# Optimization experiments

Hardware: AMD Instinct MI355X
Metric: run time of the kernel (lower is better)

Reference implementation:

```python
import jax, jax.numpy as jnp
import numpy as np

TEMP = 0.07
NEG_INF = -1e30  # finite stand-in for -inf; safe under vjp


def setup_inputs() -> dict:
    key = jax.random.key(0)
    k1, k2, k3 = jax.random.split(key, 3)
    B, D, H, F = 16384, 2048, 2048, 128  # 2N rows, backbone_dim, hidden_dim, feature_dim
    features = jax.random.normal(k1, (B, D), dtype=jnp.float32)
    w1 = jax.random.normal(k2, (D, H), dtype=jnp.float32) / np.sqrt(D)
    b1 = jnp.zeros((H,), dtype=jnp.float32)
    w2 = jax.random.normal(k3, (H, F), dtype=jnp.float32) / np.sqrt(H)
    b2 = jnp.zeros((F,), dtype=jnp.float32)
    return {"features": features, "w1": w1, "b1": b1, "w2": w2, "b2": b2}


def reference(features, w1, b1, w2, b2):
    # Projector: Linear -> ReLU -> Linear, then L2-normalize (F.normalize, dim=1)
    h = jax.nn.relu(features @ w1 + b1)
    p = h @ w2 + b2
    z = p / jnp.maximum(jnp.linalg.norm(p, axis=1, keepdims=True), 1e-12)

    M = z.shape[0]           # 2N
    N = M // 2
    sim = (z @ z.T) / TEMP   # [2N, 2N]

    # NT-Xent with labels=0: loss_i = logsumexp_{j != i}(sim[i,j]) - pos_i
    # (pos appears exactly once among the logits, so the gather loop over
    #  per-row negatives collapses to a diagonal-masked row logsumexp).
    diag = jnp.eye(M, dtype=bool)
    lse = jax.nn.logsumexp(jnp.where(diag, NEG_INF, sim), axis=1)
    pos = jnp.sum(z * jnp.roll(z, N, axis=0), axis=1) / TEMP  # sim[i, (i+N) % 2N]
    loss = jnp.mean(lse - pos)
    return loss, z[:N], z[N:]
```

## Files before the change

### kernel.cpp

```cpp
#include <hip/hip_runtime.h>

typedef __attribute__((ext_vector_type(8))) __bf16 bf16x8;
typedef __attribute__((ext_vector_type(4))) float f32x4;

#define B_ROWS 16384
#define N_HALF 8192
#define D_DIM  2048
#define H_DIM  2048
#define F_DIM  128

static constexpr float kInvT = 14.285714285714286f;
static constexpr float kS2   = 20.60992915555662f;

__device__ __forceinline__ void async16(void* lds, const void* g) {
  __builtin_amdgcn_global_load_lds((const __attribute__((address_space(1))) void*)g,
                                   (__attribute__((address_space(3))) void*)lds,
                                   16, 0, 0);
}

__global__ void cvt_bf16_kernel(const float* __restrict__ in, __bf16* __restrict__ out, int n) {
  int i = (blockIdx.x * blockDim.x + threadIdx.x) * 8;
  if (i >= n) return;
  float4 a = *(const float4*)(in + i);
  float4 b = *(const float4*)(in + i + 4);
  bf16x8 o;
  o[0] = (__bf16)a.x; o[1] = (__bf16)a.y; o[2] = (__bf16)a.z; o[3] = (__bf16)a.w;
  o[4] = (__bf16)b.x; o[5] = (__bf16)b.y; o[6] = (__bf16)b.z; o[7] = (__bf16)b.w;
  *(bf16x8*)(out + i) = o;
}

__global__ void transpose_cvt_kernel(const float* __restrict__ in, __bf16* __restrict__ out,
                                     int R, int C) {
  __shared__ float tile[32][33];
  int tx = threadIdx.x, ty = threadIdx.y;
  int c0 = blockIdx.x * 32, r0 = blockIdx.y * 32;
  for (int i = 0; i < 4; i++)
    tile[ty + i * 8][tx] = in[(size_t)(r0 + ty + i * 8) * C + c0 + tx];
  __syncthreads();
  for (int i = 0; i < 4; i++)
    out[(size_t)(c0 + ty + i * 8) * R + r0 + tx] = (__bf16)tile[tx][ty + i * 8];
}

#define BM 256
#define BK 64
#define NT_K (D_DIM / BK)

__global__ __launch_bounds__(512, 2) void gemm1_8ph_kernel(
    const __bf16* __restrict__ A, const __bf16* __restrict__ BT,
    const float* __restrict__ bias, __bf16* __restrict__ C) {
  __shared__ __align__(16) __bf16 As[2][BM * BK];
  __shared__ __align__(16) __bf16 Bs[2][BM * BK];
  const int t = threadIdx.x;
  const int wave = t >> 6, lane = t & 63;
  const int l15 = lane & 15, quad = lane >> 4, l7 = l15 & 7;
  const int wy = wave & 1, wx = wave >> 1;

  const int wg = ((int)blockIdx.x & 7) * 64 + ((int)blockIdx.x >> 3);
  const int n0 = (wg & 7) * 256;
  const int m0 = (wg >> 3) * 256;

  const int tr = t >> 3;
  const int csw = ((t & 7) ^ (tr & 7)) * 8;
  const __bf16* pA = A + (size_t)(m0 + tr) * D_DIM + csw;
  const __bf16* pB = BT + (size_t)(n0 + tr) * D_DIM + csw;
  const int ldsw = wave * 512;

  auto stageA = [&](int buf, int h, int kk) {
    async16(&As[buf][h * 8192 + ldsw], pA + (size_t)(h * 128) * D_DIM + kk);
    async16(&As[buf][h * 8192 + 4096 + ldsw], pA + (size_t)(h * 128 + 64) * D_DIM + kk);
  };
  auto stageB = [&](int buf, int h, int kk) {
    async16(&Bs[buf][h * 8192 + ldsw], pB + (size_t)(h * 128) * D_DIM + kk);
    async16(&Bs[buf][h * 8192 + 4096 + ldsw], pB + (size_t)(h * 128 + 64) * D_DIM + kk);
  };

  const int arow = wy * 16 + l15;
  const int brow = wx * 16 + l15;
  const int s0 = (quad ^ l7) * 8;
  const int s1 = ((4 + quad) ^ l7) * 8;

  f32x4 acc[8][4];
#pragma unroll
  for (int f = 0; f < 8; f++)
#pragma unroll
    for (int n = 0; n < 4; n++) acc[f][n] = 0.f;

  stageB(0, 0, 0); stageB(0, 1, 0);
  stageA(0, 0, 0); stageA(0, 1, 0);
  stageB(1, 0, BK); stageB(1, 1, BK);
  asm volatile("s_waitcnt vmcnt(4)" ::: "memory");
  __builtin_amdgcn_s_barrier();

  for (int tk = 0; tk < NT_K; ++tk) {
    const int cur = tk & 1, nxt = cur ^ 1;
    const __bf16* Ac = &As[cur][0];
    const __bf16* Bc = &Bs[cur][0];
#define LDA(f, s) (*(const bf16x8*)(Ac + ((f) * 32 + arow) * 64 + (s)))
#define LDB(n, s) (*(const bf16x8*)(Bc + ((n) * 64 + brow) * 64 + (s)))
    bf16x8 b0[4], b1[4];
    {
      bf16x8 a0 = LDA(0, s0), a1 = LDA(1, s0), a2 = LDA(2, s0), a3 = LDA(3, s0);
      b0[0] = LDB(0, s0); b0[1] = LDB(1, s0); b0[2] = LDB(2, s0); b0[3] = LDB(3, s0);
      if (tk + 1 < NT_K) stageA(nxt, 0, (tk + 1) * BK);
      __builtin_amdgcn_s_barrier();
      asm volatile("s_waitcnt lgkmcnt(0)" ::: "memory");
      __builtin_amdgcn_s_setprio(1);
#pragma unroll
      for (int n = 0; n < 4; n++) {
        acc[0][n] = __builtin_amdgcn_mfma_f32_16x16x32_bf16(a0, b0[n], acc[0][n], 0, 0, 0);
        acc[1][n] = __builtin_amdgcn_mfma_f32_16x16x32_bf16(a1, b0[n], acc[1][n], 0, 0, 0);
        acc[2][n] = __builtin_amdgcn_mfma_f32_16x16x32_bf16(a2, b0[n], acc[2][n], 0, 0, 0);
        acc[3][n] = __builtin_amdgcn_mfma_f32_16x16x32_bf16(a3, b0[n], acc[3][n], 0, 0, 0);
      }
      __builtin_amdgcn_s_setprio(0);
      __builtin_amdgcn_s_barrier();
    }
    {
      bf16x8 a4 = LDA(4, s0), a5 = LDA(5, s0), a6 = LDA(6, s0), a7 = LDA(7, s0);
      if (tk + 1 < NT_K) stageA(nxt, 1, (tk + 1) * BK);
      __builtin_amdgcn_s_barrier();
      asm volatile("s_waitcnt lgkmcnt(0)" ::: "memory");
      __builtin_amdgcn_s_setprio(1);
#pragma unroll
      for (int n = 0; n < 4; n++) {
        acc[4][n] = __builtin_amdgcn_mfma_f32_16x16x32_bf16(a4, b0[n], acc[4][n], 0, 0, 0);
        acc[5][n] = __builtin_amdgcn_mfma_f32_16x16x32_bf16(a5, b0[n], acc[5][n], 0, 0, 0);
        acc[6][n] = __builtin_amdgcn_mfma_f32_16x16x32_bf16(a6, b0[n], acc[6][n], 0, 0, 0);
        acc[7][n] = __builtin_amdgcn_mfma_f32_16x16x32_bf16(a7, b0[n], acc[7][n], 0, 0, 0);
      }
      __builtin_amdgcn_s_setprio(0);
      __builtin_amdgcn_s_barrier();
    }
    {
      bf16x8 a0 = LDA(0, s1), a1 = LDA(1, s1), a2 = LDA(2, s1), a3 = LDA(3, s1);
      b1[0] = LDB(0, s1); b1[1] = LDB(1, s1); b1[2] = LDB(2, s1); b1[3] = LDB(3, s1);
      __builtin_amdgcn_s_barrier();
      asm volatile("s_waitcnt lgkmcnt(0)" ::: "memory");
      __builtin_amdgcn_s_setprio(1);
#pragma unroll
      for (int n = 0; n < 4; n++) {
        acc[0][n] = __builtin_amdgcn_mfma_f32_16x16x32_bf16(a0, b1[n], acc[0][n], 0, 0, 0);
        acc[1][n] = __builtin_amdgcn_mfma_f32_16x16x32_bf16(a1, b1[n], acc[1][n], 0, 0, 0);
        acc[2][n] = __builtin_amdgcn_mfma_f32_16x16x32_bf16(a2, b1[n], acc[2][n], 0, 0, 0);
        acc[3][n] = __builtin_amdgcn_mfma_f32_16x16x32_bf16(a3, b1[n], acc[3][n], 0, 0, 0);
      }
      __builtin_amdgcn_s_setprio(0);
      __builtin_amdgcn_s_barrier();
    }
    {
      bf16x8 a4 = LDA(4, s1), a5 = LDA(5, s1), a6 = LDA(6, s1), a7 = LDA(7, s1);
      if (tk + 2 < NT_K) {
        stageB(cur, 0, (tk + 2) * BK);
        stageB(cur, 1, (tk + 2) * BK);
        asm volatile("s_waitcnt vmcnt(4)" ::: "memory");
      } else if (tk + 1 < NT_K) {
        asm volatile("s_waitcnt vmcnt(0)" ::: "memory");
      }
      __builtin_amdgcn_s_barrier();
      asm volatile("s_waitcnt lgkmcnt(0)" ::: "memory");
      __builtin_amdgcn_s_setprio(1);
#pragma unroll
      for (int n = 0; n < 4; n++) {
        acc[4][n] = __builtin_amdgcn_mfma_f32_16x16x32_bf16(a4, b1[n], acc[4][n], 0, 0, 0);
        acc[5][n] = __builtin_amdgcn_mfma_f32_16x16x32_bf16(a5, b1[n], acc[5][n], 0, 0, 0);
        acc[6][n] = __builtin_amdgcn_mfma_f32_16x16x32_bf16(a6, b1[n], acc[6][n], 0, 0, 0);
        acc[7][n] = __builtin_amdgcn_mfma_f32_16x16x32_bf16(a7, b1[n], acc[7][n], 0, 0, 0);
      }
      __builtin_amdgcn_s_setprio(0);
      __builtin_amdgcn_s_barrier();
    }
#undef LDA
#undef LDB
  }

#pragma unroll
  for (int n = 0; n < 4; n++) {
    int col = n0 + n * 64 + wx * 16 + l15;
    float bv = bias[col];
#pragma unroll
    for (int f = 0; f < 8; f++) {
      int rowb = m0 + f * 32 + wy * 16 + quad * 4;
#pragma unroll
      for (int r = 0; r < 4; r++) {
        float v = fmaxf(acc[f][n][r] + bv, 0.f);
        C[(size_t)(rowb + r) * H_DIM + col] = (__bf16)v;
      }
    }
  }
}

__global__ __launch_bounds__(256) void proj_norm_kernel(
    const __bf16* __restrict__ A, const __bf16* __restrict__ BT,
    const float* __restrict__ bias, float* __restrict__ zf, __bf16* __restrict__ zb, int K) {
  __shared__ __align__(16) __bf16 As[64 * 32];
  __shared__ __align__(16) __bf16 Bs[128 * 32];
  __shared__ float pbuf[64 * 128];
  const int t = threadIdx.x;
  const int wave = t >> 6, lane = t & 63;
  const int l15 = lane & 15, quad = lane >> 4;
  const int wy = wave >> 1, wx = wave & 1;
  const int m0 = blockIdx.x * 64;
  const int sr = t >> 2;
  const int sk = (((t & 3) ^ ((sr >> 1) & 3))) * 8;
  const int sw = (l15 >> 1) & 3;

  f32x4 acc[2][4];
  for (int i = 0; i < 2; i++)
    for (int j = 0; j < 4; j++) acc[i][j] = 0.f;

  for (int k0 = 0; k0 < K; k0 += 32) {
    async16(As + wave * 512, A + (size_t)(m0 + sr) * K + k0 + sk);
    async16(Bs + 0 * 2048 + wave * 512, BT + (size_t)(0  + sr) * K + k0 + sk);
    async16(Bs + 1 * 2048 + wave * 512, BT + (size_t)(64 + sr) * K + k0 + sk);
    __syncthreads();
    bf16x8 af[2], bfr[4];
    for (int i = 0; i < 2; i++)
      af[i] = *(const bf16x8*)(As + (wy * 32 + i * 16 + l15) * 32 + (quad ^ sw) * 8);
    for (int i = 0; i < 4; i++)
      bfr[i] = *(const bf16x8*)(Bs + (wx * 64 + i * 16 + l15) * 32 + (quad ^ sw) * 8);
    for (int mi = 0; mi < 2; mi++)
      for (int ni = 0; ni < 4; ni++)
        acc[mi][ni] = __builtin_amdgcn_mfma_f32_16x16x32_bf16(af[mi], bfr[ni], acc[mi][ni], 0, 0, 0);
    __syncthreads();
  }
  for (int ni = 0; ni < 4; ni++) {
    int col = wx * 64 + ni * 16 + l15;
    float bv = bias[col];
    for (int mi = 0; mi < 2; mi++) {
      int lrow = wy * 32 + mi * 16 + quad * 4;
      for (int r = 0; r < 4; r++)
        pbuf[(lrow + r) * 128 + col] = acc[mi][ni][r] + bv;
    }
  }
  __syncthreads();
  for (int it = 0; it < 16; it++) {
    int lrow = wave * 16 + it;
    float v0 = pbuf[lrow * 128 + lane];
    float v1 = pbuf[lrow * 128 + 64 + lane];
    float ss = v0 * v0 + v1 * v1;
    for (int m = 1; m < 64; m <<= 1) ss += __shfl_xor(ss, m);
    float inv = 1.f / fmaxf(sqrtf(ss), 1e-12f);
    float z0 = v0 * inv, z1 = v1 * inv;
    size_t base = (size_t)(m0 + lrow) * F_DIM;
    zf[base + lane] = z0;
    zf[base + 64 + lane] = z1;
    zb[base + lane] = (__bf16)z0;
    zb[base + 64 + lane] = (__bf16)z1;
  }
}

__global__ __launch_bounds__(256) void sim_lse_tri_kernel(const __bf16* __restrict__ zb,
                                                          float* __restrict__ S,
                                                          float* __restrict__ colpart) {
  __shared__ __align__(16) __bf16 Bs[128 * 128];
  const int t = threadIdx.x;
  const int wave = t >> 6, lane = t & 63;
  const int l15 = lane & 15, quad = lane >> 4;
  const int wy = wave >> 1, wx = wave & 1;
  const int srow = t >> 4;
  const int schunk = (t & 15) ^ srow;

  const int u = blockIdx.x * 8;
  auto fr = [](int r) { return r * 128 - (r * (r - 1)) / 2; };
  int rt = (int)(128.5f - sqrtf(16512.25f - 2.0f * (float)u));
  while (fr(rt + 1) <= u) rt++;
  while (fr(rt) > u) rt--;
  int ct = rt + (u - fr(rt));

  bf16x8 a[4][4];
  float rowacc[4][4];
  auto load_a = [&](int rtile) {
#pragma unroll
    for (int mi = 0; mi < 4; mi++)
#pragma unroll
      for (int ks = 0; ks < 4; ks++)
        a[mi][ks] = *(const bf16x8*)(zb + (size_t)(rtile * 128 + wy * 64 + mi * 16 + l15) * 128 +
                                     ks * 32 + quad * 8);
  };
  auto flush_rows = [&](int rtile) {
#pragma unroll
    for (int mi = 0; mi < 4; mi++)
#pragma unroll
      for (int r = 0; r < 4; r++) {
        float v = rowacc[mi][r];
        v += __shfl_xor(v, 1);
        v += __shfl_xor(v, 2);
        v += __shfl_xor(v, 4);
        v += __shfl_xor(v, 8);
        if (l15 == 0)
          atomicAdd(&S[rtile * 128 + wy * 64 + mi * 16 + quad * 4 + r], v);
        rowacc[mi][r] = 0.f;
      }
  };

#pragma unroll
  for (int mi = 0; mi < 4; mi++)
#pragma unroll
    for (int r = 0; r < 4; r++) rowacc[mi][r] = 0.f;
  load_a(rt);

  for (int it = 0; it < 8; ++it) {
    const __bf16* gbase = zb + (size_t)(ct * 128) * 128;
#pragma unroll
    for (int q = 0; q < 8; q++)
      async16(Bs + q * 2048 + wave * 512, gbase + (size_t)(q * 16 + srow) * 128 + schunk * 8);
    __syncthreads();
    const bool diag = (ct == rt);
#pragma unroll
    for (int ni = 0; ni < 4; ni++) {
      bf16x8 b[4];
      const int brow = wx * 64 + ni * 16 + l15;
#pragma unroll
      for (int ks = 0; ks < 4; ks++)
        b[ks] = *(const bf16x8*)(Bs + brow * 128 + (((ks * 4 + quad) ^ l15) * 8));
      float colsum = 0.f;
      if (diag) {
#pragma unroll
        for (int mi = 0; mi < 4; mi++) {
          f32x4 acc = 0.f;
#pragma unroll
          for (int ks = 0; ks < 4; ks++)
            acc = __builtin_amdgcn_mfma_f32_16x16x32_bf16(a[mi][ks], b[ks], acc, 0, 0, 0);
          const int lrb = wy * 64 + mi * 16 + quad * 4;
#pragma unroll
          for (int r = 0; r < 4; r++) {
            float term = __builtin_amdgcn_exp2f(fmaf(acc[r], kS2, -kS2));
            rowacc[mi][r] += (lrb + r == brow) ? 0.f : term;
          }
        }
      } else {
#pragma unroll
        for (int mi = 0; mi < 4; mi++) {
          f32x4 acc = 0.f;
#pragma unroll
          for (int ks = 0; ks < 4; ks++)
            acc = __builtin_amdgcn_mfma_f32_16x16x32_bf16(a[mi][ks], b[ks], acc, 0, 0, 0);
#pragma unroll
          for (int r = 0; r < 4; r++) {
            float term = __builtin_amdgcn_exp2f(fmaf(acc[r], kS2, -kS2));
            rowacc[mi][r] += term;
            colsum += term;
          }
        }
        colsum += __shfl_xor(colsum, 16);
        colsum += __shfl_xor(colsum, 32);
        if (quad == 0)
          colpart[((size_t)(ct * 128 + rt) * 2 + wy) * 128 + brow] = colsum;
      }
    }
    __syncthreads();
    if (it < 7) {
      ct++;
      if (ct == 128) {
        flush_rows(rt);
        rt++;
        ct = rt;
        load_a(rt);
      }
    }
  }
  flush_rows(rt);
}

__global__ __launch_bounds__(128) void col_reduce_kernel(const float* __restrict__ colpart,
                                                         float* __restrict__ S) {
  const int ct = blockIdx.y;
  const int r0 = blockIdx.x * 32;
  if (r0 >= ct) return;
  const int t = threadIdx.x;
  const int rend = min(ct, r0 + 32);
  float s = 0.f;
  for (int rt = r0; rt < rend; rt++) {
    const float* p = colpart + (size_t)(ct * 128 + rt) * 2 * 128;
    s += p[t] + p[128 + t];
  }
  atomicAdd(&S[ct * 128 + t], s);
}

__global__ void loss_kernel(const float* __restrict__ zf, const float* __restrict__ S,
                            float* __restrict__ out) {
  int wave = threadIdx.x >> 6, lane = threadIdx.x & 63;
  int base = blockIdx.x * 64 + wave * 16;
  float local = 0.f;
  for (int it = 0; it < 16; it++) {
    int row = base + it;
    int j = (row + N_HALF) & (B_ROWS - 1);
    const float* za = zf + (size_t)row * F_DIM;
    const float* zc = zf + (size_t)j * F_DIM;
    float d = za[lane] * zc[lane] + za[lane + 64] * zc[lane + 64];
    for (int m = 1; m < 64; m <<= 1) d += __shfl_xor(d, m);
    float pos = d * kInvT;
    float lse = logf(S[row]) + kInvT;
    local += (lse - pos);
  }
  if (lane == 0) atomicAdd(out, local * (1.f / B_ROWS));
}

extern "C" void kernel_launch(void* const* d_in, const int* in_sizes, int n_in,
                              void* d_out, int out_size, void* d_ws, size_t ws_size,
                              hipStream_t stream) {
  const float* features = (const float*)d_in[0];
  const float* w1 = (const float*)d_in[1];
  const float* b1 = (const float*)d_in[2];
  const float* w2 = (const float*)d_in[3];
  const float* b2 = (const float*)d_in[4];
  float* out = (float*)d_out;

  char* ws = (char*)d_ws;
  size_t off = 0;
  __bf16* A1  = (__bf16*)(ws + off); off += (size_t)B_ROWS * D_DIM * 2;
  __bf16* h   = (__bf16*)(ws + off); off += (size_t)B_ROWS * H_DIM * 2;
  __bf16* w1t = (__bf16*)(ws + off); off += (size_t)H_DIM * D_DIM * 2;
  __bf16* w2t = (__bf16*)(ws + off); off += (size_t)F_DIM * H_DIM * 2;
  __bf16* zbb = (__bf16*)(ws + off); off += (size_t)B_ROWS * F_DIM * 2;
  float*  S   = (float*)(ws + off);  off += (size_t)B_ROWS * 4;
  float* colpart = (float*)A1;

  hipMemsetAsync(S, 0, (size_t)B_ROWS * 4, stream);
  hipMemsetAsync(out, 0, 4, stream);

  {
    int n = B_ROWS * D_DIM;
    cvt_bf16_kernel<<<n / (256 * 8), 256, 0, stream>>>(features, A1, n);
  }
  transpose_cvt_kernel<<<dim3(H_DIM / 32, D_DIM / 32), dim3(32, 8), 0, stream>>>(w1, w1t, D_DIM, H_DIM);
  transpose_cvt_kernel<<<dim3(F_DIM / 32, H_DIM / 32), dim3(32, 8), 0, stream>>>(w2, w2t, H_DIM, F_DIM);

  gemm1_8ph_kernel<<<dim3((B_ROWS / 256) * (H_DIM / 256)), 512, 0, stream>>>(A1, w1t, b1, h);

  proj_norm_kernel<<<B_ROWS / 64, 256, 0, stream>>>(h, w2t, b2, out + 1, zbb, H_DIM);

  sim_lse_tri_kernel<<<1032, 256, 0, stream>>>(zbb, S, colpart);
  col_reduce_kernel<<<dim3(4, 128), 128, 0, stream>>>(colpart, S);

  loss_kernel<<<B_ROWS / 64, 256, 0, stream>>>(out + 1, S, out);
}
```

Measured before the change: 488.1 us.

## Pipeline projector GEMM loads, defer gemm1 vmcnt wait, rebalance similarity tiles

In the projector GEMM, the single-buffer load/sync loop becomes a 5-deep ring of LDS buffers with four stages prefetched ahead and explicit vmcnt waits, so global-to-LDS latency can overlap with MFMA work. In gemm1, the vmcnt wait for the next B stage moves after the second MFMA block so the loads overlap more compute. The triangular similarity kernel now spreads the 8256 tiles evenly over 1024 blocks (about 8 each) instead of 1032 blocks of exactly 8. The costs are more LDS per block for the projector, which may lower occupancy, and hand-counted wait counts that must match the issued loads.

```diff
diff --git a/kernel.cpp b/kernel.cpp
--- a/kernel.cpp
+++ b/kernel.cpp
@@ -149,12 +149,10 @@
     }
     {
       bf16x8 a4 = LDA(4, s1), a5 = LDA(5, s1), a6 = LDA(6, s1), a7 = LDA(7, s1);
-      if (tk + 2 < NT_K) {
+      const bool st = (tk + 2 < NT_K);
+      if (st) {
         stageB(cur, 0, (tk + 2) * BK);
         stageB(cur, 1, (tk + 2) * BK);
-        asm volatile("s_waitcnt vmcnt(4)" ::: "memory");
-      } else if (tk + 1 < NT_K) {
-        asm volatile("s_waitcnt vmcnt(0)" ::: "memory");
       }
       __builtin_amdgcn_s_barrier();
       asm volatile("s_waitcnt lgkmcnt(0)" ::: "memory");
@@ -167,6 +165,11 @@
         acc[7][n] = __builtin_amdgcn_mfma_f32_16x16x32_bf16(a7, b1[n], acc[7][n], 0, 0, 0);
       }
       __builtin_amdgcn_s_setprio(0);
+      if (st) {
+        asm volatile("s_waitcnt vmcnt(4)" ::: "memory");
+      } else if (tk + 1 < NT_K) {
+        asm volatile("s_waitcnt vmcnt(0)" ::: "memory");
+      }
       __builtin_amdgcn_s_barrier();
     }
 #undef LDA
@@ -192,8 +195,8 @@
 __global__ __launch_bounds__(256) void proj_norm_kernel(
     const __bf16* __restrict__ A, const __bf16* __restrict__ BT,
     const float* __restrict__ bias, float* __restrict__ zf, __bf16* __restrict__ zb, int K) {
-  __shared__ __align__(16) __bf16 As[64 * 32];
-  __shared__ __align__(16) __bf16 Bs[128 * 32];
+  __shared__ __align__(16) __bf16 As[5 * 64 * 32];
+  __shared__ __align__(16) __bf16 Bs[5 * 128 * 32];
   __shared__ float pbuf[64 * 128];
   const int t = threadIdx.x;
   const int wave = t >> 6, lane = t & 63;
@@ -203,26 +206,46 @@
   const int sr = t >> 2;
   const int sk = (((t & 3) ^ ((sr >> 1) & 3))) * 8;
   const int sw = (l15 >> 1) & 3;
+  const int NK = K / 32;
+
+  auto stage = [&](int buf, int k0) {
+    async16(As + buf * 2048 + wave * 512, A + (size_t)(m0 + sr) * K + k0 + sk);
+    async16(Bs + buf * 4096 + wave * 512, BT + (size_t)(0  + sr) * K + k0 + sk);
+    async16(Bs + buf * 4096 + 2048 + wave * 512, BT + (size_t)(64 + sr) * K + k0 + sk);
+  };
 
   f32x4 acc[2][4];
   for (int i = 0; i < 2; i++)
     for (int j = 0; j < 4; j++) acc[i][j] = 0.f;
 
-  for (int k0 = 0; k0 < K; k0 += 32) {
-    async16(As + wave * 512, A + (size_t)(m0 + sr) * K + k0 + sk);
-    async16(Bs + 0 * 2048 + wave * 512, BT + (size_t)(0  + sr) * K + k0 + sk);
-    async16(Bs + 1 * 2048 + wave * 512, BT + (size_t)(64 + sr) * K + k0 + sk);
-    __syncthreads();
+  stage(0, 0); stage(1, 32); stage(2, 64); stage(3, 96);
+  asm volatile("s_waitcnt vmcnt(9)" ::: "memory");
+  __builtin_amdgcn_s_barrier();
+
+  for (int kk = 0; kk < NK; ++kk) {
+    const int cur = kk % 5;
     bf16x8 af[2], bfr[4];
     for (int i = 0; i < 2; i++)
-      af[i] = *(const bf16x8*)(As + (wy * 32 + i * 16 + l15) * 32 + (quad ^ sw) * 8);
+      af[i] = *(const bf16x8*)(As + cur * 2048 + (wy * 32 + i * 16 + l15) * 32 + (quad ^ sw) * 8);
     for (int i = 0; i < 4; i++)
-      bfr[i] = *(const bf16x8*)(Bs + (wx * 64 + i * 16 + l15) * 32 + (quad ^ sw) * 8);
+      bfr[i] = *(const bf16x8*)(Bs + cur * 4096 + (wx * 64 + i * 16 + l15) * 32 + (quad ^ sw) * 8);
+    if (kk + 4 < NK) stage((kk + 4) % 5, (kk + 4) * 32);
+    asm volatile("s_waitcnt lgkmcnt(0)" ::: "memory");
+    if (kk + 4 < NK) {
+      asm volatile("s_waitcnt vmcnt(9)" ::: "memory");
+    } else if (kk == NK - 4) {
+      asm volatile("s_waitcnt vmcnt(6)" ::: "memory");
+    } else if (kk == NK - 3) {
+      asm volatile("s_waitcnt vmcnt(3)" ::: "memory");
+    } else {
+      asm volatile("s_waitcnt vmcnt(0)" ::: "memory");
+    }
+    __builtin_amdgcn_s_barrier();
     for (int mi = 0; mi < 2; mi++)
       for (int ni = 0; ni < 4; ni++)
         acc[mi][ni] = __builtin_amdgcn_mfma_f32_16x16x32_bf16(af[mi], bfr[ni], acc[mi][ni], 0, 0, 0);
-    __syncthreads();
-  }
+  }
+  __syncthreads();
   for (int ni = 0; ni < 4; ni++) {
     int col = wx * 64 + ni * 16 + l15;
     float bv = bias[col];
@@ -260,12 +283,14 @@
   const int srow = t >> 4;
   const int schunk = (t & 15) ^ srow;
 
-  const int u = blockIdx.x * 8;
+  const int u0 = (int)(((long)blockIdx.x * 8256) >> 10);
+  const int u1 = (int)(((long)(blockIdx.x + 1) * 8256) >> 10);
+
   auto fr = [](int r) { return r * 128 - (r * (r - 1)) / 2; };
-  int rt = (int)(128.5f - sqrtf(16512.25f - 2.0f * (float)u));
-  while (fr(rt + 1) <= u) rt++;
-  while (fr(rt) > u) rt--;
-  int ct = rt + (u - fr(rt));
+  int rt = (int)(128.5f - sqrtf(16512.25f - 2.0f * (float)u0));
+  while (fr(rt + 1) <= u0) rt++;
+  while (fr(rt) > u0) rt--;
+  int ct = rt + (u0 - fr(rt));
 
   bf16x8 a[4][4];
   float rowacc[4][4];
@@ -299,7 +324,7 @@
     for (int r = 0; r < 4; r++) rowacc[mi][r] = 0.f;
   load_a(rt);
 
-  for (int it = 0; it < 8; ++it) {
+  for (int u = u0; u < u1; ++u) {
     const __bf16* gbase = zb + (size_t)(ct * 128) * 128;
 #pragma unroll
     for (int q = 0; q < 8; q++)
@@ -349,7 +374,7 @@
       }
     }
     __syncthreads();
-    if (it < 7) {
+    if (u + 1 < u1) {
       ct++;
       if (ct == 128) {
         flush_rows(rt);
@@ -430,7 +455,7 @@
 
   proj_norm_kernel<<<B_ROWS / 64, 256, 0, stream>>>(h, w2t, b2, out + 1, zbb, H_DIM);
 
-  sim_lse_tri_kernel<<<1032, 256, 0, stream>>>(zbb, S, colpart);
+  sim_lse_tri_kernel<<<1024, 256, 0, stream>>>(zbb, S, colpart);
   col_reduce_kernel<<<dim3(4, 128), 128, 0, stream>>>(colpart, S);
 
   loss_kernel<<<B_ROWS / 64, 256, 0, stream>>>(out + 1, S, out);
```

New measurement: 482.3 us. About the same (-1.2%).
